# Performance work log

Measured on AMD Instinct MI355X. Metric: run time of the kernel, lower is better.

## Reference

```python
import jax, jax.numpy as jnp
import numpy as np

BANDWIDTH = 1.0  # init kwarg: bandwidth; sphere mode -> var_s = gamma = bandwidth
LOG2PI = float(np.log(2.0 * np.pi))


def setup_inputs() -> dict:
    key = jax.random.key(0)
    k1, k2, k3, k4 = jax.random.split(key, 4)
    x = jax.random.normal(k1, (4096, 256), dtype=jnp.float32)
    y = jax.random.normal(k2, (4096, 128), dtype=jnp.float32)
    x_s = jax.random.normal(k3, (8192, 256), dtype=jnp.float32)
    y_s = jax.random.normal(k4, (8192, 128), dtype=jnp.float32)
    return {"x": x, "y": y, "x_s": x_s, "y_s": y_s}


def _sq_dists(a, b):
    # ||a_i - b_j||^2 via GEMM expansion: (batch, num_s)
    a2 = jnp.sum(a * a, axis=-1)[:, None]
    b2 = jnp.sum(b * b, axis=-1)[None, :]
    return a2 + b2 - 2.0 * jnp.einsum("bd,sd->bs", a, b)


def reference(x, y, x_s, y_s):
    x_dim = x.shape[-1]
    y_dim = y.shape[-1]
    var_s = BANDWIDTH
    gamma = BANDWIDTH
    logA_x = x_dim * (LOG2PI + jnp.log(jnp.float32(var_s)))
    logA_y = y_dim * (LOG2PI + jnp.log(jnp.float32(gamma)))

    sdx = _sq_dists(x, x_s) / var_s  # (batch, num_s)
    sdy = _sq_dists(y, y_s) / gamma  # (batch, num_s)

    E_log_pxy = jax.nn.logsumexp(-0.5 * (logA_x + logA_y + sdx + sdy), axis=-1)
    E_log_px = jax.nn.logsumexp(-0.5 * (logA_x + sdx), axis=-1)
    E_log_py = jax.nn.logsumexp(-0.5 * (logA_y + sdy), axis=-1)
    return jnp.mean(E_log_pxy - E_log_px - E_log_py)
```

## Files before the change

kernel.cpp:

```cpp
#include <hip/hip_runtime.h>
#include <hip/hip_bf16.h>
#include <stdint.h>

#define B_N 4096
#define S_N 8192
#define KX  256
#define KY  128
#define BM 128
#define BN 128

typedef __bf16 bf16x8 __attribute__((ext_vector_type(8)));
typedef float  f32x4  __attribute__((ext_vector_type(4)));

#define OFF_XH   ((size_t)0)
#define OFF_YH   ((size_t)2097152)
#define OFF_SXH  ((size_t)3145728)
#define OFF_SYH  ((size_t)7340032)
#define OFF_NX   ((size_t)9437184)
#define OFF_NY   (OFF_NX + 16384)
#define OFF_NSX  (OFF_NY + 16384)
#define OFF_NSY  (OFF_NSX + 32768)
#define OFF_PART (OFF_NSY + 32768)
#define OFF_BSUM (OFF_PART + (size_t)3*64*4096*2*4)

__device__ __forceinline__ void gl2lds16(const void* g, void* l) {
  typedef const __attribute__((address_space(1))) unsigned int* gp_t;
  typedef __attribute__((address_space(3))) unsigned int* lp_t;
  __builtin_amdgcn_global_load_lds((gp_t)g, (lp_t)l, 16, 0, 0);
}

__device__ __forceinline__ unsigned short f2bf(float f) {
  unsigned u = __builtin_bit_cast(unsigned, f);
  return (unsigned short)((u + 0x7fffu + ((u >> 16) & 1u)) >> 16);
}

__global__ __launch_bounds__(256) void conv_all(const float* __restrict__ x,
                                                const float* __restrict__ y,
                                                const float* __restrict__ xs,
                                                const float* __restrict__ ys,
                                                char* __restrict__ ws) {
  int b    = blockIdx.x;
  int wave = threadIdx.x >> 6;
  int lane = threadIdx.x & 63;
  const float* src; unsigned short* hi; float* nrm;
  int K, row;
  if (b < 1024) {
    src = x;  hi = (unsigned short*)(ws + OFF_XH);
    nrm = (float*)(ws + OFF_NX); K = 256; row = b * 4 + wave;
  } else if (b < 2048) {
    src = y;  hi = (unsigned short*)(ws + OFF_YH);
    nrm = (float*)(ws + OFF_NY); K = 128; row = (b - 1024) * 4 + wave;
  } else if (b < 4096) {
    src = xs; hi = (unsigned short*)(ws + OFF_SXH);
    nrm = (float*)(ws + OFF_NSX); K = 256; row = (b - 2048) * 4 + wave;
  } else {
    src = ys; hi = (unsigned short*)(ws + OFF_SYH);
    nrm = (float*)(ws + OFF_NSY); K = 128; row = (b - 4096) * 4 + wave;
  }
  float acc = 0.f;
  if (K == 256) {
    float4 v = ((const float4*)(src + (size_t)row * 256))[lane];
    float vv[4] = {v.x, v.y, v.z, v.w};
    ushort4 h4;
    unsigned short* hp = (unsigned short*)&h4;
    #pragma unroll
    for (int k = 0; k < 4; ++k) {
      hp[k] = f2bf(vv[k]);
      acc = fmaf(vv[k], vv[k], acc);
    }
    ((ushort4*)(hi + (size_t)row * 256))[lane] = h4;
  } else {
    float2 v = ((const float2*)(src + (size_t)row * 128))[lane];
    float vv[2] = {v.x, v.y};
    ushort2 h2;
    unsigned short* hp = (unsigned short*)&h2;
    #pragma unroll
    for (int k = 0; k < 2; ++k) {
      hp[k] = f2bf(vv[k]);
      acc = fmaf(vv[k], vv[k], acc);
    }
    ((ushort2*)(hi + (size_t)row * 128))[lane] = h2;
  }
  #pragma unroll
  for (int o = 32; o > 0; o >>= 1) acc += __shfl_down(acc, o);
  if (lane == 0) nrm[row] = acc;
}

__global__ __launch_bounds__(512, 4) void mie_main(const char* __restrict__ ws,
                                                   float* __restrict__ part) {
  __shared__ __align__(16) char smem[32768];

  const int tid  = threadIdx.x;
  const int lane = tid & 63;
  const int wave = tid >> 6;
  const int c    = lane & 15;
  const int q    = lane >> 4;
  const int wm   = wave >> 1;
  const int wn   = wave & 1;

  const int b     = blockIdx.x;
  const int xcd   = b & 7;
  const int w     = b >> 3;
  const int bm_t  = w & 31;
  const int sn_t  = xcd * 8 + (w >> 5);
  const int bm0   = bm_t * BM;
  const int sn0   = sn_t * BN;

  const char* xh  = ws + OFF_XH;
  const char* yh  = ws + OFF_YH;
  const char* sxh = ws + OFF_SXH;
  const char* syh = ws + OFF_SYH;
  const float* nx  = (const float*)(ws + OFF_NX);
  const float* ny  = (const float*)(ws + OFF_NY);
  const float* nsx = (const float*)(ws + OFF_NSX);
  const float* nsy = (const float*)(ws + OFF_NSY);

  auto stage = [&](int kc, int buf) {
    const char *ah, *bh; int rb, k0b;
    if (kc < 8) { ah = xh; bh = sxh; rb = 512; k0b = kc * 64; }
    else        { ah = yh; bh = syh; rb = 256; k0b = (kc - 8) * 64; }
    char* base = smem + buf * 16384;
    int l  = wave * 64 + lane;
    int r  = l >> 2;
    int sl = l & 3;
    int g  = sl ^ ((r >> 1) & 3);
    size_t kofs = (size_t)k0b + (size_t)g * 16;
    size_t goA  = (size_t)(bm0 + r) * rb + kofs;
    size_t goB  = (size_t)(sn0 + r) * rb + kofs;
    char* dst = base + wave * 1024;
    gl2lds16(ah + goA, dst);
    gl2lds16(bh + goB, dst + 8192);
  };

  const int slot = (q ^ ((c >> 1) & 3)) * 16;
  int aoff[2], boff[4];
  #pragma unroll
  for (int i = 0; i < 2; ++i) aoff[i] = (wm * 32 + i * 16 + c) * 64 + slot;
  #pragma unroll
  for (int j = 0; j < 4; ++j) boff[j] = (wn * 64 + j * 16 + c) * 64 + slot;

  f32x4 accx[2][4], accy[2][4];
  #pragma unroll
  for (int i = 0; i < 2; ++i)
    #pragma unroll
    for (int j = 0; j < 4; ++j) {
      accx[i][j] = (f32x4){0.f,0.f,0.f,0.f};
      accy[i][j] = (f32x4){0.f,0.f,0.f,0.f};
    }

  stage(0, 0);
  __syncthreads();

  for (int kc = 0; kc < 12; ++kc) {
    if (kc < 11) stage(kc + 1, (kc + 1) & 1);
    const char* base = smem + (kc & 1) * 16384;
    bf16x8 Ah[2], Bh[4];
    #pragma unroll
    for (int i = 0; i < 2; ++i) Ah[i] = *(const bf16x8*)(base + aoff[i]);
    #pragma unroll
    for (int j = 0; j < 4; ++j) Bh[j] = *(const bf16x8*)(base + 8192 + boff[j]);
    if (kc < 8) {
      #pragma unroll
      for (int i = 0; i < 2; ++i)
        #pragma unroll
        for (int j = 0; j < 4; ++j)
          accx[i][j] = __builtin_amdgcn_mfma_f32_16x16x32_bf16(Ah[i], Bh[j], accx[i][j], 0, 0, 0);
    } else {
      #pragma unroll
      for (int i = 0; i < 2; ++i)
        #pragma unroll
        for (int j = 0; j < 4; ++j)
          accy[i][j] = __builtin_amdgcn_mfma_f32_16x16x32_bf16(Ah[i], Bh[j], accy[i][j], 0, 0, 0);
    }
    __syncthreads();
  }

  float hxv[2][4], hyv[2][4];
  #pragma unroll
  for (int i = 0; i < 2; ++i)
    #pragma unroll
    for (int r = 0; r < 4; ++r) {
      int rr = bm0 + wm * 32 + i * 16 + q * 4 + r;
      hxv[i][r] = -0.5f * nx[rr];
      hyv[i][r] = -0.5f * ny[rr];
    }
  float hsxv[4], hsyv[4];
  #pragma unroll
  for (int j = 0; j < 4; ++j) {
    int cc = sn0 + wn * 64 + j * 16 + c;
    hsxv[j] = -0.5f * nsx[cc];
    hsyv[j] = -0.5f * nsy[cc];
  }

  float2* xch = (float2*)smem;
  #pragma unroll
  for (int i = 0; i < 2; ++i) {
    #pragma unroll
    for (int r = 0; r < 4; ++r) {
      float vx[4], vy[4];
      #pragma unroll
      for (int j = 0; j < 4; ++j) {
        vx[j] = accx[i][j][r] + hxv[i][r] + hsxv[j];
        vy[j] = accy[i][j][r] + hyv[i][r] + hsyv[j];
      }
      int rl = wm * 32 + i * 16 + q * 4 + r;
      #pragma unroll
      for (int st = 0; st < 3; ++st) {
        float v0 = (st == 0) ? vx[0] + vy[0] : (st == 1 ? vx[0] : vy[0]);
        float v1 = (st == 0) ? vx[1] + vy[1] : (st == 1 ? vx[1] : vy[1]);
        float v2 = (st == 0) ? vx[2] + vy[2] : (st == 1 ? vx[2] : vy[2]);
        float v3 = (st == 0) ? vx[3] + vy[3] : (st == 1 ? vx[3] : vy[3]);
        float m = fmaxf(fmaxf(v0, v1), fmaxf(v2, v3));
        #pragma unroll
        for (int msk = 1; msk < 16; msk <<= 1) m = fmaxf(m, __shfl_xor(m, msk));
        float s = __expf(v0 - m) + __expf(v1 - m) + __expf(v2 - m) + __expf(v3 - m);
        #pragma unroll
        for (int msk = 1; msk < 16; msk <<= 1) s += __shfl_xor(s, msk);
        if (c == 0) xch[(st * 128 + rl) * 2 + wn] = (float2){m, s};
      }
    }
  }
  __syncthreads();

  if (tid < 384) {
    int st = tid >> 7;
    int rl = tid & 127;
    float2 a = xch[(st * 128 + rl) * 2 + 0];
    float2 bb = xch[(st * 128 + rl) * 2 + 1];
    float m = fmaxf(a.x, bb.x);
    float s = a.y * __expf(a.x - m) + bb.y * __expf(bb.x - m);
    size_t idx = ((size_t)st * 64 + sn_t) * B_N + (bm0 + rl);
    ((float2*)part)[idx] = (float2){m, s};
  }
}

__global__ __launch_bounds__(256) void fin1(const float* __restrict__ part,
                                            float* __restrict__ bsum) {
  __shared__ float2 lds[3][4][64];
  int tid  = threadIdx.x;
  int wave = tid >> 6;
  int lane = tid & 63;
  int row  = blockIdx.x * 64 + lane;
  #pragma unroll
  for (int j = 0; j < 3; ++j) {
    float m = -__builtin_inff(), s = 0.f;
    #pragma unroll
    for (int pp = 0; pp < 16; ++pp) {
      int p = wave * 16 + pp;
      float2 a = ((const float2*)part)[((size_t)j * 64 + p) * B_N + row];
      float nm = fmaxf(m, a.x);
      s = s * __expf(m - nm) + a.y * __expf(a.x - nm);
      m = nm;
    }
    lds[j][wave][lane] = (float2){m, s};
  }
  __syncthreads();
  if (wave == 0) {
    float v[3];
    #pragma unroll
    for (int j = 0; j < 3; ++j) {
      float m = -__builtin_inff(), s = 0.f;
      #pragma unroll
      for (int u = 0; u < 4; ++u) {
        float2 a = lds[j][u][lane];
        float nm = fmaxf(m, a.x);
        s = s * __expf(m - nm) + a.y * __expf(a.x - nm);
        m = nm;
      }
      v[j] = m + __logf(s);
    }
    float local = v[0] - v[1] - v[2];
    #pragma unroll
    for (int o = 32; o > 0; o >>= 1) local += __shfl_down(local, o);
    if (lane == 0) bsum[blockIdx.x] = local;
  }
}

__global__ void fin2(const float* __restrict__ bsum, float* __restrict__ out) {
  int t = threadIdx.x;
  float a = bsum[t];
  #pragma unroll
  for (int o = 32; o > 0; o >>= 1) a += __shfl_down(a, o);
  if (t == 0) out[0] = a * (1.0f / (float)B_N);
}

extern "C" void kernel_launch(void* const* d_in, const int* in_sizes, int n_in,
                              void* d_out, int out_size, void* d_ws, size_t ws_size,
                              hipStream_t stream) {
  (void)in_sizes; (void)n_in; (void)out_size; (void)ws_size;
  const float* x  = (const float*)d_in[0];
  const float* y  = (const float*)d_in[1];
  const float* xs = (const float*)d_in[2];
  const float* ys = (const float*)d_in[3];
  char* ws = (char*)d_ws;

  conv_all<<<6144, 256, 0, stream>>>(x, y, xs, ys, ws);
  mie_main<<<2048, 512, 0, stream>>>(ws, (float*)(ws + OFF_PART));
  fin1<<<B_N / 64, 256, 0, stream>>>((const float*)(ws + OFF_PART), (float*)(ws + OFF_BSUM));
  fin2<<<1, 64, 0, stream>>>((const float*)(ws + OFF_BSUM), (float*)d_out);
}
```

Measured before the change: 146.2 us.

## Deepen GEMM pipeline to four LDS buffers with explicit vmcnt waits

```diff
diff --git a/kernel.cpp b/kernel.cpp
--- a/kernel.cpp
+++ b/kernel.cpp
@@ -88,7 +88,7 @@
 
 __global__ __launch_bounds__(512, 4) void mie_main(const char* __restrict__ ws,
                                                    float* __restrict__ part) {
-  __shared__ __align__(16) char smem[32768];
+  __shared__ __align__(16) char smem[65536];
 
   const int tid  = threadIdx.x;
   const int lane = tid & 63;
@@ -115,29 +115,21 @@
   const float* nsx = (const float*)(ws + OFF_NSX);
   const float* nsy = (const float*)(ws + OFF_NSY);
 
-  auto stage = [&](int kc, int buf) {
-    const char *ah, *bh; int rb, k0b;
-    if (kc < 8) { ah = xh; bh = sxh; rb = 512; k0b = kc * 64; }
-    else        { ah = yh; bh = syh; rb = 256; k0b = (kc - 8) * 64; }
-    char* base = smem + buf * 16384;
-    int l  = wave * 64 + lane;
-    int r  = l >> 2;
-    int sl = l & 3;
-    int g  = sl ^ ((r >> 1) & 3);
-    size_t kofs = (size_t)k0b + (size_t)g * 16;
-    size_t goA  = (size_t)(bm0 + r) * rb + kofs;
-    size_t goB  = (size_t)(sn0 + r) * rb + kofs;
-    char* dst = base + wave * 1024;
-    gl2lds16(ah + goA, dst);
-    gl2lds16(bh + goB, dst + 8192);
-  };
-
-  const int slot = (q ^ ((c >> 1) & 3)) * 16;
-  int aoff[2], boff[4];
-  #pragma unroll
-  for (int i = 0; i < 2; ++i) aoff[i] = (wm * 32 + i * 16 + c) * 64 + slot;
-  #pragma unroll
-  for (int j = 0; j < 4; ++j) boff[j] = (wn * 64 + j * 16 + c) * 64 + slot;
+  const int r  = tid >> 2;
+  const int sg = (tid & 3) ^ ((r >> 1) & 3);
+  const char* aXp = xh  + (size_t)(bm0 + r) * 512 + sg * 16;
+  const char* aYp = yh  + (size_t)(bm0 + r) * 256 + sg * 16;
+  const char* bXp = sxh + (size_t)(sn0 + r) * 512 + sg * 16;
+  const char* bYp = syh + (size_t)(sn0 + r) * 256 + sg * 16;
+  char* sdst = smem + wave * 1024;
+
+  const int slot  = (q ^ ((c >> 1) & 3)) * 16;
+  const int aoff0 = (wm * 32 +  0 + c) * 64 + slot;
+  const int aoff1 = (wm * 32 + 16 + c) * 64 + slot;
+  const int boff0 = (wn * 64 +  0 + c) * 64 + slot;
+  const int boff1 = (wn * 64 + 16 + c) * 64 + slot;
+  const int boff2 = (wn * 64 + 32 + c) * 64 + slot;
+  const int boff3 = (wn * 64 + 48 + c) * 64 + slot;
 
   f32x4 accx[2][4], accy[2][4];
   #pragma unroll
@@ -148,41 +140,64 @@
       accy[i][j] = (f32x4){0.f,0.f,0.f,0.f};
     }
 
-  stage(0, 0);
-  __syncthreads();
-
-  for (int kc = 0; kc < 12; ++kc) {
-    if (kc < 11) stage(kc + 1, (kc + 1) & 1);
-    const char* base = smem + (kc & 1) * 16384;
-    bf16x8 Ah[2], Bh[4];
-    #pragma unroll
-    for (int i = 0; i < 2; ++i) Ah[i] = *(const bf16x8*)(base + aoff[i]);
-    #pragma unroll
-    for (int j = 0; j < 4; ++j) Bh[j] = *(const bf16x8*)(base + 8192 + boff[j]);
-    if (kc < 8) {
-      #pragma unroll
-      for (int i = 0; i < 2; ++i)
-        #pragma unroll
-        for (int j = 0; j < 4; ++j)
-          accx[i][j] = __builtin_amdgcn_mfma_f32_16x16x32_bf16(Ah[i], Bh[j], accx[i][j], 0, 0, 0);
-    } else {
-      #pragma unroll
-      for (int i = 0; i < 2; ++i)
-        #pragma unroll
-        for (int j = 0; j < 4; ++j)
-          accy[i][j] = __builtin_amdgcn_mfma_f32_16x16x32_bf16(Ah[i], Bh[j], accy[i][j], 0, 0, 0);
-    }
-    __syncthreads();
-  }
+#define STAGE(kc) do {                                                      \
+    const char* _sa; const char* _sb;                                       \
+    if ((kc) < 8) { _sa = aXp + (kc) * 64;       _sb = bXp + (kc) * 64; }   \
+    else          { _sa = aYp + ((kc) - 8) * 64; _sb = bYp + ((kc) - 8) * 64; } \
+    char* _d = sdst + ((kc) & 3) * 16384;                                   \
+    gl2lds16(_sa, _d);                                                      \
+    gl2lds16(_sb, _d + 8192);                                               \
+  } while (0)
+
+#define MFMA8(ACC, A0, A1, B0, B1, B2, B3) do {                                   \
+    ACC[0][0] = __builtin_amdgcn_mfma_f32_16x16x32_bf16(A0, B0, ACC[0][0], 0,0,0); \
+    ACC[0][1] = __builtin_amdgcn_mfma_f32_16x16x32_bf16(A0, B1, ACC[0][1], 0,0,0); \
+    ACC[0][2] = __builtin_amdgcn_mfma_f32_16x16x32_bf16(A0, B2, ACC[0][2], 0,0,0); \
+    ACC[0][3] = __builtin_amdgcn_mfma_f32_16x16x32_bf16(A0, B3, ACC[0][3], 0,0,0); \
+    ACC[1][0] = __builtin_amdgcn_mfma_f32_16x16x32_bf16(A1, B0, ACC[1][0], 0,0,0); \
+    ACC[1][1] = __builtin_amdgcn_mfma_f32_16x16x32_bf16(A1, B1, ACC[1][1], 0,0,0); \
+    ACC[1][2] = __builtin_amdgcn_mfma_f32_16x16x32_bf16(A1, B2, ACC[1][2], 0,0,0); \
+    ACC[1][3] = __builtin_amdgcn_mfma_f32_16x16x32_bf16(A1, B3, ACC[1][3], 0,0,0); \
+  } while (0)
+
+#define KSTEP(kc, vm, ACC) do {                                             \
+    if ((kc) + 3 < 12) STAGE((kc) + 3);                                     \
+    asm volatile("s_waitcnt vmcnt(" #vm ")" ::: "memory");                  \
+    __builtin_amdgcn_s_barrier();                                           \
+    asm volatile("" ::: "memory");                                          \
+    const char* _base = smem + ((kc) & 3) * 16384;                          \
+    bf16x8 _A0 = *(const bf16x8*)(_base + aoff0);                           \
+    bf16x8 _A1 = *(const bf16x8*)(_base + aoff1);                           \
+    bf16x8 _B0 = *(const bf16x8*)(_base + 8192 + boff0);                    \
+    bf16x8 _B1 = *(const bf16x8*)(_base + 8192 + boff1);                    \
+    bf16x8 _B2 = *(const bf16x8*)(_base + 8192 + boff2);                    \
+    bf16x8 _B3 = *(const bf16x8*)(_base + 8192 + boff3);                    \
+    __builtin_amdgcn_s_setprio(1);                                          \
+    MFMA8(ACC, _A0, _A1, _B0, _B1, _B2, _B3);                               \
+    __builtin_amdgcn_s_setprio(0);                                          \
+    asm volatile("" ::: "memory");                                          \
+    __builtin_amdgcn_s_barrier();                                           \
+    asm volatile("" ::: "memory");                                          \
+  } while (0)
+
+  STAGE(0); STAGE(1); STAGE(2);
+
+  KSTEP(0, 6, accx);  KSTEP(1, 6, accx);  KSTEP(2, 6, accx);  KSTEP(3, 6, accx);
+  KSTEP(4, 6, accx);  KSTEP(5, 6, accx);  KSTEP(6, 6, accx);  KSTEP(7, 6, accx);
+  KSTEP(8, 6, accy);  KSTEP(9, 4, accy);  KSTEP(10, 2, accy); KSTEP(11, 0, accy);
+
+#undef KSTEP
+#undef MFMA8
+#undef STAGE
 
   float hxv[2][4], hyv[2][4];
   #pragma unroll
   for (int i = 0; i < 2; ++i)
     #pragma unroll
-    for (int r = 0; r < 4; ++r) {
-      int rr = bm0 + wm * 32 + i * 16 + q * 4 + r;
-      hxv[i][r] = -0.5f * nx[rr];
-      hyv[i][r] = -0.5f * ny[rr];
+    for (int rr4 = 0; rr4 < 4; ++rr4) {
+      int rr = bm0 + wm * 32 + i * 16 + q * 4 + rr4;
+      hxv[i][rr4] = -0.5f * nx[rr];
+      hyv[i][rr4] = -0.5f * ny[rr];
     }
   float hsxv[4], hsyv[4];
   #pragma unroll
@@ -196,14 +211,14 @@
   #pragma unroll
   for (int i = 0; i < 2; ++i) {
     #pragma unroll
-    for (int r = 0; r < 4; ++r) {
+    for (int rr4 = 0; rr4 < 4; ++rr4) {
       float vx[4], vy[4];
       #pragma unroll
       for (int j = 0; j < 4; ++j) {
-        vx[j] = accx[i][j][r] + hxv[i][r] + hsxv[j];
-        vy[j] = accy[i][j][r] + hyv[i][r] + hsyv[j];
+        vx[j] = accx[i][j][rr4] + hxv[i][rr4] + hsxv[j];
+        vy[j] = accy[i][j][rr4] + hyv[i][rr4] + hsyv[j];
       }
-      int rl = wm * 32 + i * 16 + q * 4 + r;
+      int rl = wm * 32 + i * 16 + q * 4 + rr4;
       #pragma unroll
       for (int st = 0; st < 3; ++st) {
         float v0 = (st == 0) ? vx[0] + vy[0] : (st == 1 ? vx[0] : vy[0]);
```

New measurement: 145.8 us. No clear change (-0.3%).
